# Performance work log

Hardware: AMD Instinct MI355X
Metric: run time of the kernel (lower is better)

## Reference

```python
import jax, jax.numpy as jnp
import numpy as np


def _chamfer(array1, array2):
    # array1: [B, N, 3], array2: [B, M, 3]
    sq1 = jnp.sum(array1 * array1, axis=-1)            # [B, N]
    sq2 = jnp.sum(array2 * array2, axis=-1)            # [B, M]
    inner = jnp.einsum('bnd,bmd->bnm', array1, array2)  # [B, N, M]
    d = sq1[:, :, None] + sq2[:, None, :] - 2.0 * inner  # [B, N, M]
    d = jnp.maximum(d, 0.0)  # clamp tiny negatives from cancellation
    dist1 = jnp.min(d, axis=2)  # [B, N] nearest in array2 for each pt in array1
    dist2 = jnp.min(d, axis=1)  # [B, M] nearest in array1 for each pt in array2
    return dist1, dist2


def setup_inputs() -> dict:
    key = jax.random.key(0)
    k1, k2 = jax.random.split(key)
    B, N, M = 8, 4096, 4096
    array1 = jax.random.normal(k1, (B, N, 3), dtype=jnp.float32)
    array2 = jax.random.normal(k2, (B, M, 3), dtype=jnp.float32)
    return {"array1": array1, "array2": array2}


def reference(array1, array2):
    dist1, dist2 = _chamfer(array1, array2)
    return jnp.mean(dist1) + jnp.mean(dist2)
```

## Files before the change

kernel.cpp:

```cpp
#include <hip/hip_runtime.h>
#include <math.h>

#define BATCH   8
#define NPTS    4096
#define TOTAL   (BATCH * NPTS)
#define THREADS 256
#define P       8
#define TILE    (THREADS * P)
#define TILES   (TOTAL / TILE)
#define CHUNKS  32
#define CHUNK   (NPTS / CHUNKS)
#define NBLOCK  (2 * TILES * CHUNKS)


__global__ __launch_bounds__(THREADS)
void chamfer_kernel(const float* __restrict__ a1, const float* __restrict__ a2,
                    unsigned* __restrict__ dist) {
    const int bid   = blockIdx.x;
    const int dir   = bid >> 9;
    const int r     = bid & 511;
    const int tile  = r >> 5;
    const int chunk = r & 31;
    const int batch = tile >> 1;

    const float* __restrict__ sraw = dir ? a2 : a1;
    const float* __restrict__ qraw = dir ? a1 : a2;

    __shared__ float4 lq[CHUNK];
    if (threadIdx.x < CHUNK) {
        const int p = batch * NPTS + chunk * CHUNK + threadIdx.x;
        const float* __restrict__ g = qraw + 3 * p;
        float x = g[0], y = g[1], z = g[2];
        lq[threadIdx.x] = make_float4(-2.0f * x, -2.0f * y, -2.0f * z,
                                      fmaf(x, x, fmaf(y, y, z * z)));
    }

    float xs[P], ys[P], zs[P], sq[P];
    #pragma unroll
    for (int k = 0; k < P; k++) {
        int si = tile * TILE + k * THREADS + threadIdx.x;
        float x = sraw[3 * si + 0];
        float y = sraw[3 * si + 1];
        float z = sraw[3 * si + 2];
        xs[k] = x;
        ys[k] = y;
        zs[k] = z;
        sq[k] = fmaf(x, x, fmaf(y, y, z * z));
    }
    __syncthreads();

    float acc[P];
    #pragma unroll
    for (int k = 0; k < P; k++) acc[k] = __builtin_inff();

    #pragma unroll 2
    for (int j = 0; j < CHUNK; j += 2) {
        float4 q0 = lq[j];
        float4 q1 = lq[j + 1];
        #pragma unroll
        for (int k = 0; k < P; k++) {
            float d0 = fmaf(q0.x, xs[k], fmaf(q0.y, ys[k], fmaf(q0.z, zs[k], q0.w)));
            float d1 = fmaf(q1.x, xs[k], fmaf(q1.y, ys[k], fmaf(q1.z, zs[k], q1.w)));
            acc[k] = fminf(fminf(d0, d1), acc[k]);
        }
    }

    #pragma unroll
    for (int k = 0; k < P; k++) {
        int si = tile * TILE + k * THREADS + threadIdx.x;
        float dmin = fmaxf(acc[k] + sq[k], 0.0f);
        atomicMin(dist + dir * TOTAL + si, __float_as_uint(dmin));
    }
}

__global__ __launch_bounds__(1024)
void reduce_kernel(const float* __restrict__ dist, float* __restrict__ out) {
    const float4* __restrict__ dv = (const float4*)dist;
    float s = 0.0f;
    #pragma unroll
    for (int i = 0; i < (2 * TOTAL / 4) / 1024; i++) {
        float4 v = dv[i * 1024 + threadIdx.x];
        s += (v.x + v.y) + (v.z + v.w);
    }
    #pragma unroll
    for (int off = 32; off > 0; off >>= 1) s += __shfl_down(s, off, 64);
    __shared__ float wsum[16];
    if ((threadIdx.x & 63) == 0) wsum[threadIdx.x >> 6] = s;
    __syncthreads();
    if (threadIdx.x < 16) {
        float v = wsum[threadIdx.x];
        #pragma unroll
        for (int off = 8; off > 0; off >>= 1) v += __shfl_down(v, off, 16);
        if (threadIdx.x == 0) out[0] = v * (1.0f / (float)TOTAL);
    }
}

extern "C" void kernel_launch(void* const* d_in, const int* in_sizes, int n_in,
                              void* d_out, int out_size, void* d_ws, size_t ws_size,
                              hipStream_t stream) {
    const float* a1 = (const float*)d_in[0];
    const float* a2 = (const float*)d_in[1];
    float* out = (float*)d_out;

    unsigned* dist = (unsigned*)d_ws;

    chamfer_kernel<<<NBLOCK, THREADS, 0, stream>>>(a1, a2, dist);
    reduce_kernel<<<1, 1024, 0, stream>>>((const float*)dist, out);
}
```

Measured before the change: 78.77 us.

## Compute both chamfer directions from one distance pass with block column-min reduction

The kernel no longer launches separate blocks for each direction. Each block now computes a tile of pairwise distances once and derives both the row minima (kept in registers) and the column minima. Column minima are reduced through a shared-memory buffer and a 16-lane shuffle, then written with atomicMin. This halves the FMA work but adds per-phase shared-memory writes, two barriers per phase and extra min operations.

```diff
diff --git a/kernel.cpp b/kernel.cpp
--- a/kernel.cpp
+++ b/kernel.cpp
@@ -7,69 +7,91 @@
 #define THREADS 256
 #define P       8
 #define TILE    (THREADS * P)
-#define TILES   (TOTAL / TILE)
-#define CHUNKS  32
-#define CHUNK   (NPTS / CHUNKS)
-#define NBLOCK  (2 * TILES * CHUNKS)
+#define STILES  (NPTS / TILE)
+#define QCHUNK  64
+#define QCHUNKS (NPTS / QCHUNK)
+#define QSUB    16
+#define PHASES  (QCHUNK / QSUB)
+#define CPAD    272
+#define NBLOCK  (BATCH * STILES * QCHUNKS)
 
 
 __global__ __launch_bounds__(THREADS)
 void chamfer_kernel(const float* __restrict__ a1, const float* __restrict__ a2,
                     unsigned* __restrict__ dist) {
-    const int bid   = blockIdx.x;
-    const int dir   = bid >> 9;
-    const int r     = bid & 511;
-    const int tile  = r >> 5;
-    const int chunk = r & 31;
-    const int batch = tile >> 1;
+    const int bid    = blockIdx.x;
+    const int qchunk = bid & (QCHUNKS - 1);
+    const int r      = bid >> 6;
+    const int stile  = r & (STILES - 1);
+    const int batch  = r >> 1;
 
-    const float* __restrict__ sraw = dir ? a2 : a1;
-    const float* __restrict__ qraw = dir ? a1 : a2;
+    __shared__ float4 lq[QCHUNK];
+    __shared__ float  colbuf[QSUB][CPAD];
 
-    __shared__ float4 lq[CHUNK];
-    if (threadIdx.x < CHUNK) {
-        const int p = batch * NPTS + chunk * CHUNK + threadIdx.x;
-        const float* __restrict__ g = qraw + 3 * p;
+    if (threadIdx.x < QCHUNK) {
+        const int p = batch * NPTS + qchunk * QCHUNK + threadIdx.x;
+        const float* __restrict__ g = a2 + 3 * p;
         float x = g[0], y = g[1], z = g[2];
         lq[threadIdx.x] = make_float4(-2.0f * x, -2.0f * y, -2.0f * z,
                                       fmaf(x, x, fmaf(y, y, z * z)));
     }
 
-    float xs[P], ys[P], zs[P], sq[P];
+    float xs[P], ys[P], zs[P], sq[P], racc[P];
     #pragma unroll
     for (int k = 0; k < P; k++) {
-        int si = tile * TILE + k * THREADS + threadIdx.x;
-        float x = sraw[3 * si + 0];
-        float y = sraw[3 * si + 1];
-        float z = sraw[3 * si + 2];
-        xs[k] = x;
-        ys[k] = y;
-        zs[k] = z;
+        int si = batch * NPTS + stile * TILE + k * THREADS + threadIdx.x;
+        float x = a1[3 * si + 0];
+        float y = a1[3 * si + 1];
+        float z = a1[3 * si + 2];
+        xs[k] = x; ys[k] = y; zs[k] = z;
         sq[k] = fmaf(x, x, fmaf(y, y, z * z));
+        racc[k] = __builtin_inff();
     }
     __syncthreads();
 
-    float acc[P];
-    #pragma unroll
-    for (int k = 0; k < P; k++) acc[k] = __builtin_inff();
-
-    #pragma unroll 2
-    for (int j = 0; j < CHUNK; j += 2) {
-        float4 q0 = lq[j];
-        float4 q1 = lq[j + 1];
-        #pragma unroll
-        for (int k = 0; k < P; k++) {
-            float d0 = fmaf(q0.x, xs[k], fmaf(q0.y, ys[k], fmaf(q0.z, zs[k], q0.w)));
-            float d1 = fmaf(q1.x, xs[k], fmaf(q1.y, ys[k], fmaf(q1.z, zs[k], q1.w)));
-            acc[k] = fminf(fminf(d0, d1), acc[k]);
+    for (int phase = 0; phase < PHASES; ++phase) {
+        #pragma unroll 2
+        for (int jj = 0; jj < QSUB; jj += 2) {
+            const int j = phase * QSUB + jj;
+            float4 q0 = lq[j];
+            float4 q1 = lq[j + 1];
+            float c0, c1;
+            #pragma unroll
+            for (int k = 0; k < P; k++) {
+                float t0 = fmaf(q0.x, xs[k], fmaf(q0.y, ys[k], fmaf(q0.z, zs[k], q0.w)));
+                float t1 = fmaf(q1.x, xs[k], fmaf(q1.y, ys[k], fmaf(q1.z, zs[k], q1.w)));
+                racc[k] = fminf(fminf(t0, t1), racc[k]);
+                float d0 = t0 + sq[k];
+                float d1 = t1 + sq[k];
+                if (k == 0) { c0 = d0; c1 = d1; }
+                else        { c0 = fminf(c0, d0); c1 = fminf(c1, d1); }
+            }
+            colbuf[jj][threadIdx.x]     = c0;
+            colbuf[jj + 1][threadIdx.x] = c1;
         }
+        __syncthreads();
+        {
+            const int ql = threadIdx.x >> 4;
+            const int ln = threadIdx.x & 15;
+            float m = colbuf[ql][ln];
+            #pragma unroll
+            for (int i = 1; i < 16; i++) m = fminf(m, colbuf[ql][ln + 16 * i]);
+            #pragma unroll
+            for (int off = 8; off > 0; off >>= 1)
+                m = fminf(m, __shfl_xor(m, off, 16));
+            if (ln == 0) {
+                atomicMin(dist + TOTAL + batch * NPTS + qchunk * QCHUNK + phase * QSUB + ql,
+                          __float_as_uint(fmaxf(m, 0.0f)));
+            }
+        }
+        __syncthreads();
     }
 
     #pragma unroll
     for (int k = 0; k < P; k++) {
-        int si = tile * TILE + k * THREADS + threadIdx.x;
-        float dmin = fmaxf(acc[k] + sq[k], 0.0f);
-        atomicMin(dist + dir * TOTAL + si, __float_as_uint(dmin));
+        int si = stile * TILE + k * THREADS + threadIdx.x;
+        float dmin = fmaxf(racc[k] + sq[k], 0.0f);
+        atomicMin(dist + batch * NPTS + si, __float_as_uint(dmin));
     }
 }
 
```

New measurement: 75.20 us. 4.5% less time.
